# Optimization experiments

Hardware: AMD Instinct MI355X
Metric: run time of the kernel (lower is better)

Reference implementation:

```python
import jax, jax.numpy as jnp
import numpy as np

B, T, V, K = 8, 256, 16, 8
L_SRL, L_VN = 66, 40  # PropBank / VerbNet label inventory sizes


def setup_inputs() -> dict:
    key = jax.random.key(0)
    ks = jax.random.split(key, 7)
    log_srl = jax.random.normal(ks[0], (B, T, T, L_SRL), jnp.float32)
    log_vn = jax.random.normal(ks[1], (B, T, T, L_VN), jnp.float32)
    v_label = jax.random.randint(ks[2], (B, V), 0, T)          # predicate token positions
    v_l = jax.random.randint(ks[3], (B,), 1, V + 1)            # num predicates per example
    orig_l = jax.random.randint(ks[4], (B,), T // 2, T + 1)    # original seq lengths
    semlink = jax.random.randint(ks[5], (B, V, 2, K), 0, L_VN) # [.,.,0,:]=srl label ids, [.,.,1,:]=vn label ids
    semlink_l = jax.random.randint(ks[6], (B, V), 0, K + 1)    # num semlink constraints per predicate
    return {"log_srl": log_srl, "log_vn": log_vn, "v_label": v_label,
            "v_l": v_l, "orig_l": orig_l, "semlink": semlink, "semlink_l": semlink_l}


def reference(log_srl, log_vn, v_label, v_l, orig_l, semlink, semlink_l):
    # log_srl: [B,T,T,L_srl], log_vn: [B,T,T,L_vn]
    Bn, Tn = log_srl.shape[0], log_srl.shape[1]
    Vn, Kn = v_label.shape[1], semlink.shape[-1]
    b = jnp.arange(Bn)[:, None]
    # Gather predicate rows: [B,V,T,L]
    sel_srl = log_srl[b, v_label]
    sel_vn = log_vn[b, v_label]
    # batch_index1_select: gather along label axis with semlink label ids -> [B,V,T,K]
    r_idx = semlink[:, :, 0, :]  # [B,V,K]
    a_idx = semlink[:, :, 1, :]
    g_r = jnp.take_along_axis(sel_srl, r_idx[:, :, None, :], axis=3)
    g_a = jnp.take_along_axis(sel_vn, a_idx[:, :, None, :], axis=3)
    diff = jnp.abs(g_r - g_a)  # [B,V,T,K]
    # masks: semlink length (len_to_mask), valid predicates, valid tokens (:orig_l)
    k_mask = jnp.arange(Kn)[None, None, :] < semlink_l[:, :, None]   # [B,V,K]
    v_mask = jnp.arange(Vn)[None, :] < v_l[:, None]                  # [B,V]
    t_mask = jnp.arange(Tn)[None, :] < orig_l[:, None]               # [B,T]
    mask = (k_mask[:, :, None, :] & v_mask[:, :, None, None] & t_mask[:, None, :, None])
    loss = jnp.sum(jnp.where(mask, diff, 0.0))
    num_prop = jnp.sum(v_l).astype(log_srl.dtype)  # use_gold_predicate == 1 normalizer
    return loss / num_prop
```

## Files before the change

kernel.cpp:

```cpp
#include <hip/hip_runtime.h>

#define Bn   8
#define Tn   256
#define Vn   16
#define Kn   8
#define LSRL 66
#define LVN  40

__global__ __launch_bounds__(256)
void semlink_partial_kernel(const float* __restrict__ log_srl,
                            const float* __restrict__ log_vn,
                            const int*   __restrict__ v_label,
                            const int*   __restrict__ v_l,
                            const int*   __restrict__ orig_l,
                            const int*   __restrict__ semlink,
                            const int*   __restrict__ semlink_l,
                            float*       __restrict__ partials) {
    const int bv = blockIdx.x;
    const int b  = bv / Vn;
    const int v  = bv % Vn;
    const int t  = threadIdx.x;

    __shared__ int s_r[Kn];
    __shared__ int s_a[Kn];
    __shared__ int s_meta[4];

    if (t < Kn) {
        s_r[t] = semlink[(((size_t)b * Vn + v) * 2 + 0) * Kn + t];
        s_a[t] = semlink[(((size_t)b * Vn + v) * 2 + 1) * Kn + t];
    }
    if (t == 0) {
        s_meta[0] = v_label[b * Vn + v];
        s_meta[1] = semlink_l[b * Vn + v];
        s_meta[2] = v_l[b];
        s_meta[3] = orig_l[b];
    }
    __syncthreads();

    const int label = s_meta[0];
    const int sl    = s_meta[1];
    const int vl    = s_meta[2];
    const int ol    = s_meta[3];

    float local = 0.0f;
    if (v < vl && t < ol) {
        const size_t row = ((size_t)b * Tn + label) * Tn + t;
        const float* srl_row = log_srl + row * LSRL;
        const float* vn_row  = log_vn  + row * LVN;
        #pragma unroll
        for (int k = 0; k < Kn; ++k) {
            if (k < sl) {
                local += fabsf(srl_row[s_r[k]] - vn_row[s_a[k]]);
            }
        }
    }

    __shared__ float red[256];
    red[t] = local;
    __syncthreads();
    #pragma unroll
    for (int s = 128; s > 0; s >>= 1) {
        if (t < s) red[t] += red[t + s];
        __syncthreads();
    }
    if (t == 0) partials[bv] = red[0];
}

__global__ __launch_bounds__(128)
void semlink_finalize_kernel(const float* __restrict__ partials,
                             const int*   __restrict__ v_l,
                             float*       __restrict__ out) {
    const int t = threadIdx.x;
    __shared__ float red[128];
    red[t] = partials[t];
    __syncthreads();
    #pragma unroll
    for (int s = 64; s > 0; s >>= 1) {
        if (t < s) red[t] += red[t + s];
        __syncthreads();
    }
    if (t == 0) {
        int np = 0;
        #pragma unroll
        for (int b = 0; b < Bn; ++b) np += v_l[b];
        out[0] = red[0] / (float)np;
    }
}

extern "C" void kernel_launch(void* const* d_in, const int* in_sizes, int n_in,
                              void* d_out, int out_size, void* d_ws, size_t ws_size,
                              hipStream_t stream) {
    const float* log_srl   = (const float*)d_in[0];
    const float* log_vn    = (const float*)d_in[1];
    const int*   v_label   = (const int*)d_in[2];
    const int*   v_l       = (const int*)d_in[3];
    const int*   orig_l    = (const int*)d_in[4];
    const int*   semlink   = (const int*)d_in[5];
    const int*   semlink_l = (const int*)d_in[6];
    float* out = (float*)d_out;
    float* partials = (float*)d_ws;

    semlink_partial_kernel<<<Bn * Vn, 256, 0, stream>>>(
        log_srl, log_vn, v_label, v_l, orig_l, semlink, semlink_l, partials);
    semlink_finalize_kernel<<<1, 128, 0, stream>>>(partials, v_l, out);
}
```

Baseline: 11.63 us.

## Fuse partial and finalize kernels via cooperative grid sync with wave-shuffle reductions

Replaces the two-kernel scheme (per-(b,v) partial sums, then a single-block finalize) with one cooperative kernel that writes partials, performs a grid-wide sync, and has block 0 reduce them. The shared-memory tree reduction is also replaced by 64-lane shuffle reductions plus a 4-entry shared array. The aim is to remove the second kernel launch and several block barriers, at the cost of cooperative launch overhead and a grid barrier across 128 blocks.

```diff
diff --git a/kernel.cpp b/kernel.cpp
--- a/kernel.cpp
+++ b/kernel.cpp
@@ -1,4 +1,7 @@
 #include <hip/hip_runtime.h>
+#include <hip/hip_cooperative_groups.h>
+
+namespace cg = cooperative_groups;
 
 #define Bn   8
 #define Tn   256
@@ -8,30 +11,33 @@
 #define LVN  40
 
 __global__ __launch_bounds__(256)
-void semlink_partial_kernel(const float* __restrict__ log_srl,
-                            const float* __restrict__ log_vn,
-                            const int*   __restrict__ v_label,
-                            const int*   __restrict__ v_l,
-                            const int*   __restrict__ orig_l,
-                            const int*   __restrict__ semlink,
-                            const int*   __restrict__ semlink_l,
-                            float*       __restrict__ partials) {
+void semlink_fused_kernel(const float* __restrict__ log_srl,
+                          const float* __restrict__ log_vn,
+                          const int*   __restrict__ v_label,
+                          const int*   __restrict__ v_l,
+                          const int*   __restrict__ orig_l,
+                          const int*   __restrict__ semlink,
+                          const int*   __restrict__ semlink_l,
+                          float*       __restrict__ partials,
+                          float*       __restrict__ out) {
     const int bv = blockIdx.x;
-    const int b  = bv / Vn;
-    const int v  = bv % Vn;
+    const int b  = bv >> 4;
+    const int v  = bv & 15;
     const int t  = threadIdx.x;
+    const int lane = t & 63;
+    const int wid  = t >> 6;
 
     __shared__ int s_r[Kn];
     __shared__ int s_a[Kn];
     __shared__ int s_meta[4];
 
     if (t < Kn) {
-        s_r[t] = semlink[(((size_t)b * Vn + v) * 2 + 0) * Kn + t];
-        s_a[t] = semlink[(((size_t)b * Vn + v) * 2 + 1) * Kn + t];
+        s_r[t] = semlink[((bv * 2) + 0) * Kn + t];
+        s_a[t] = semlink[((bv * 2) + 1) * Kn + t];
     }
     if (t == 0) {
-        s_meta[0] = v_label[b * Vn + v];
-        s_meta[1] = semlink_l[b * Vn + v];
+        s_meta[0] = v_label[bv];
+        s_meta[1] = semlink_l[bv];
         s_meta[2] = v_l[b];
         s_meta[3] = orig_l[b];
     }
@@ -55,35 +61,34 @@
         }
     }
 
-    __shared__ float red[256];
-    red[t] = local;
+    #pragma unroll
+    for (int off = 32; off > 0; off >>= 1) local += __shfl_down(local, off);
+
+    __shared__ float wsum[4];
+    if (lane == 0) wsum[wid] = local;
     __syncthreads();
-    #pragma unroll
-    for (int s = 128; s > 0; s >>= 1) {
-        if (t < s) red[t] += red[t + s];
-        __syncthreads();
+
+    if (t == 0) {
+        float bsum = (wsum[0] + wsum[1]) + (wsum[2] + wsum[3]);
+        __hip_atomic_store(&partials[bv], bsum, __ATOMIC_RELEASE,
+                           __HIP_MEMORY_SCOPE_AGENT);
     }
-    if (t == 0) partials[bv] = red[0];
-}
 
-__global__ __launch_bounds__(128)
-void semlink_finalize_kernel(const float* __restrict__ partials,
-                             const int*   __restrict__ v_l,
-                             float*       __restrict__ out) {
-    const int t = threadIdx.x;
-    __shared__ float red[128];
-    red[t] = partials[t];
-    __syncthreads();
-    #pragma unroll
-    for (int s = 64; s > 0; s >>= 1) {
-        if (t < s) red[t] += red[t + s];
-        __syncthreads();
-    }
-    if (t == 0) {
-        int np = 0;
+    cg::this_grid().sync();
+
+    if (bv == 0 && t < 64) {
+        float x = __hip_atomic_load(&partials[t],      __ATOMIC_RELAXED,
+                                    __HIP_MEMORY_SCOPE_AGENT)
+                + __hip_atomic_load(&partials[t + 64], __ATOMIC_RELAXED,
+                                    __HIP_MEMORY_SCOPE_AGENT);
         #pragma unroll
-        for (int b = 0; b < Bn; ++b) np += v_l[b];
-        out[0] = red[0] / (float)np;
+        for (int off = 32; off > 0; off >>= 1) x += __shfl_down(x, off);
+        if (t == 0) {
+            int np = 0;
+            #pragma unroll
+            for (int bb = 0; bb < Bn; ++bb) np += v_l[bb];
+            out[0] = x / (float)np;
+        }
     }
 }
 
@@ -97,10 +102,14 @@
     const int*   orig_l    = (const int*)d_in[4];
     const int*   semlink   = (const int*)d_in[5];
     const int*   semlink_l = (const int*)d_in[6];
-    float* out = (float*)d_out;
+    float* out      = (float*)d_out;
     float* partials = (float*)d_ws;
 
-    semlink_partial_kernel<<<Bn * Vn, 256, 0, stream>>>(
-        log_srl, log_vn, v_label, v_l, orig_l, semlink, semlink_l, partials);
-    semlink_finalize_kernel<<<1, 128, 0, stream>>>(partials, v_l, out);
+    void* args[] = {
+        (void*)&log_srl, (void*)&log_vn, (void*)&v_label, (void*)&v_l,
+        (void*)&orig_l, (void*)&semlink, (void*)&semlink_l,
+        (void*)&partials, (void*)&out
+    };
+    hipLaunchCooperativeKernel((void*)semlink_fused_kernel,
+                               dim3(Bn * Vn), dim3(Tn), args, 0, stream);
 }
```

New measurement: 42.48 us. 3.65x slower.
